# Optimization experiments

Measured on AMD Instinct MI355X. Metric: run time of the kernel, lower is better.

## Reference

```python
import jax, jax.numpy as jnp
import numpy as np

B, N, D, E = 4, 1024, 1024, 8
TOP_N = 2
THRESHOLD = 0.2
EPS = 1e-9
CAP_FACTOR = 2.0
MIN_EXPERT_CAPACITY = 4
H = int(D * 4 * 2 / 3)  # GEGLU hidden = 2730


def setup_inputs() -> dict:
    key = jax.random.key(0)
    ks = jax.random.split(key, 8)
    u = lambda k, shape, fan: jax.random.uniform(k, shape, jnp.float32, -1.0, 1.0) * (fan ** -0.5)
    return {
        "x": jax.random.normal(ks[0], (B, N, D), jnp.float32),
        "route_probs": jax.random.uniform(ks[1], (TOP_N, B, N), jnp.float32),
        "gate_w": u(ks[2], (D, E), D),
        "w1": u(ks[3], (E, D, 2 * H), 2 * H),
        "b1": u(ks[4], (E, 2 * H), 2 * H),
        "mult_bias": jnp.ones((E, H), jnp.float32),
        "w2": u(ks[5], (E, H, D), D),
        "b2": u(ks[6], (E, D), D),
    }


def reference(x, route_probs, gate_w, w1, b1, mult_bias, w2, b2):
    b, n, d = x.shape
    e = gate_w.shape[1]
    cap = max(min(n, int(n * CAP_FACTOR / e)), MIN_EXPERT_CAPACITY)  # 256

    # ---- top-n gating ----
    logits = jnp.einsum('bnd,de->bne', x, gate_w)
    raw_gates = jax.nn.softmax(logits, axis=-1)
    gate_vals, gate_idx = jax.lax.top_k(raw_gates, TOP_N)          # [b,n,k]
    gate_vals = jnp.moveaxis(gate_vals, -1, 0)                      # [k,b,n]
    gate_idx = jnp.moveaxis(gate_idx, -1, 0)                        # [k,b,n]
    one_hot_idx = jax.nn.one_hot(gate_idx, e, dtype=x.dtype)        # [k,b,n,e]

    denom = jnp.clip(gate_vals.sum(axis=0, keepdims=True), EPS)
    gate_vals = gate_vals / denom

    # route to expert k>0 with prob min(1, gate/threshold); expert 0 always routed
    should_route = route_probs < (gate_vals / THRESHOLD)
    should_route = should_route.at[0].set(True)
    mask = one_hot_idx * should_route[..., None].astype(x.dtype)    # [k,b,n,e]

    # exclusive cumsum over sequence dim -> position within each expert
    mask_cumsum = jnp.cumsum(mask, axis=2) - mask                   # [k,b,n,e]

    positions, masks = [], []
    prev_count = jnp.zeros((b, 1, e), x.dtype)
    for k in range(TOP_N):  # small fixed loop over top-n
        pos_e = (mask_cumsum[k] + prev_count) * mask[k]             # [b,n,e]
        mk = mask[k] * (pos_e < float(cap)).astype(x.dtype)
        prev_count = prev_count + mk.sum(axis=1, keepdims=True)
        positions.append(pos_e.sum(axis=-1))                        # [b,n]
        masks.append(mk)
    positions = jnp.stack(positions)                                # [k,b,n]
    mask = jnp.stack(masks)                                         # [k,b,n,e]

    mask_flat = mask.sum(axis=-1)                                   # [k,b,n] in {0,1}
    gates = gate_vals * mask_flat
    pos_one_hot = jax.nn.one_hot(positions.astype(jnp.int32), cap, dtype=x.dtype)  # [k,b,n,c]

    # combine tensor [b,n,e,c]; dispatch is its boolean support
    combine = jnp.einsum('kbn,kbne,kbnc->bnec', gates * mask_flat, one_hot_idx, pos_one_hot)
    dispatch = (combine > 0).astype(x.dtype)

    # ---- dispatch tokens to experts ----
    xe = jnp.einsum('bnd,bnec->ebcd', x, dispatch)                  # [e,b,c,d]

    # ---- per-expert GEGLU FFN (grouped GEMM) ----
    h = jnp.einsum('ebcd,edf->ebcf', xe, w1) + b1[:, None, None, :]
    val, gate = jnp.split(h, 2, axis=-1)
    act = jax.nn.gelu(gate, approximate=False) * val * mult_bias[:, None, None, :]
    out_e = jnp.einsum('ebch,ehd->ebcd', act, w2) + b2[:, None, None, :]

    # ---- combine ----
    out = jnp.einsum('ebcd,bnec->bnd', out_e, combine)
    return out


if __name__ == '__main__':
    inp = setup_inputs()
    o = reference(**inp)
    print(o.shape, o.dtype)
```

## Files before the change

### kernel.cpp

```cpp
#include <hip/hip_runtime.h>
#include <hip/hip_bf16.h>
#include <math.h>

#define B_ 4
#define N_ 1024
#define D_ 1024
#define E_ 8
#define H_ 2730
#define H2_ 5460
#define CAP_ 256
#define NTOK 4096
#define NSLOT 8192
#define NKT1 16
#define NKT2 43
#define NFG 22

typedef __attribute__((ext_vector_type(8))) short short8;
typedef __attribute__((ext_vector_type(4))) float f32x4;

__device__ __forceinline__ unsigned short f2bf(float f) {
    __hip_bfloat16 h = __float2bfloat16(f);
    return *reinterpret_cast<unsigned short*>(&h);
}
__device__ __forceinline__ float bf2f(unsigned short u) {
    unsigned x = ((unsigned)u) << 16;
    union { unsigned u; float f; } c; c.u = x; return c.f;
}

#define GLL16(g, l)                                                          \
    __builtin_amdgcn_global_load_lds(                                        \
        (const __attribute__((address_space(1))) void*)(g),                  \
        (__attribute__((address_space(3))) void*)(l), 16, 0, 0)

#define VMCNT4() asm volatile("s_waitcnt vmcnt(4)" ::: "memory")
#define VMCNT3() asm volatile("s_waitcnt vmcnt(3)" ::: "memory")
#define VMCNT0() asm volatile("s_waitcnt vmcnt(0)" ::: "memory")
#define SBAR()   __builtin_amdgcn_s_barrier()
#define SCHEDB() __builtin_amdgcn_sched_barrier(0)
#define MFMA16(a, b, c) __builtin_amdgcn_mfma_f32_16x16x32_bf16((a), (b), (c), 0, 0, 0)


__global__ __launch_bounds__(256) void k_cvt1(const float* __restrict__ w1,
                                              unsigned short* __restrict__ w1p) {
    const int fg = blockIdx.x;
    const int kt = blockIdx.y;
    const int e  = blockIdx.z;
    const float* w1e = w1 + (size_t)e * D_ * H2_;
    unsigned short* dst = w1p + (((size_t)((e * NFG + fg) * NKT1 + kt)) << 14);
#pragma unroll
    for (int i = 0; i < 8; ++i) {
        const int o = i * 256 + threadIdx.x;
        const int l = o & 63, n16 = (o >> 6) & 15, k32 = o >> 10;
        const int f = fg * 128 + ((n16 & 7) << 4) + (l & 15);
        const int k = kt * 64 + (k32 << 5) + ((l >> 4) << 3);
        ushort4 r0 = {0, 0, 0, 0}, r1 = {0, 0, 0, 0};
        if (f < H_) {
            const float* s = w1e + (size_t)k * H2_ + (n16 >= 8 ? H_ : 0) + f;
            r0.x = f2bf(s[0]);
            r0.y = f2bf(s[(size_t)H2_]);
            r0.z = f2bf(s[(size_t)2 * H2_]);
            r0.w = f2bf(s[(size_t)3 * H2_]);
            r1.x = f2bf(s[(size_t)4 * H2_]);
            r1.y = f2bf(s[(size_t)5 * H2_]);
            r1.z = f2bf(s[(size_t)6 * H2_]);
            r1.w = f2bf(s[(size_t)7 * H2_]);
        }
        *reinterpret_cast<ushort4*>(dst + (size_t)o * 8) = r0;
        *reinterpret_cast<ushort4*>(dst + (size_t)o * 8 + 4) = r1;
    }
}

__global__ __launch_bounds__(256) void k_cvt2(const float* __restrict__ w2,
                                              unsigned short* __restrict__ w2p) {
    const int kt = blockIdx.x;
    const int nt = blockIdx.y;
    const int e  = blockIdx.z;
    const float* w2e = w2 + (size_t)e * H_ * D_;
    unsigned short* dst = w2p + (((size_t)((e * 8 + nt) * NKT2 + kt)) << 13);
#pragma unroll
    for (int i = 0; i < 4; ++i) {
        const int o = i * 256 + threadIdx.x;
        const int l = o & 63, n16 = (o >> 6) & 7, k32 = o >> 9;
        const int d = nt * 128 + (n16 << 4) + (l & 15);
        const int f = kt * 64 + (k32 << 5) + ((l >> 4) << 3);
        const float* s = w2e + (size_t)f * D_ + d;
        ushort4 r0, r1;
        r0.x = (f + 0 < H_) ? f2bf(s[0]) : 0;
        r0.y = (f + 1 < H_) ? f2bf(s[(size_t)D_]) : 0;
        r0.z = (f + 2 < H_) ? f2bf(s[(size_t)2 * D_]) : 0;
        r0.w = (f + 3 < H_) ? f2bf(s[(size_t)3 * D_]) : 0;
        r1.x = (f + 4 < H_) ? f2bf(s[(size_t)4 * D_]) : 0;
        r1.y = (f + 5 < H_) ? f2bf(s[(size_t)5 * D_]) : 0;
        r1.z = (f + 6 < H_) ? f2bf(s[(size_t)6 * D_]) : 0;
        r1.w = (f + 7 < H_) ? f2bf(s[(size_t)7 * D_]) : 0;
        *reinterpret_cast<ushort4*>(dst + (size_t)o * 8) = r0;
        *reinterpret_cast<ushort4*>(dst + (size_t)o * 8 + 4) = r1;
    }
}

__global__ __launch_bounds__(256) void k_gate(const float* __restrict__ x,
                                              const float* __restrict__ route,
                                              const float* __restrict__ gw,
                                              int* __restrict__ tokE,
                                              float* __restrict__ tokG,
                                              int* __restrict__ tokR) {
    const int wave = threadIdx.x >> 6, lane = threadIdx.x & 63;
    const int t = blockIdx.x * 4 + wave;
    float acc[E_];
#pragma unroll
    for (int e = 0; e < E_; ++e) acc[e] = 0.f;
    const float* xr = x + (size_t)t * D_;
    for (int d = lane; d < D_; d += 64) {
        float xv = xr[d];
        const float* g = gw + d * E_;
#pragma unroll
        for (int e = 0; e < E_; ++e) acc[e] = fmaf(xv, g[e], acc[e]);
    }
#pragma unroll
    for (int e = 0; e < E_; ++e) {
#pragma unroll
        for (int off = 32; off; off >>= 1) acc[e] += __shfl_xor(acc[e], off);
    }
    if (lane == 0) {
        float m = acc[0];
#pragma unroll
        for (int e = 1; e < E_; ++e) m = fmaxf(m, acc[e]);
        float p[E_]; float s = 0.f;
#pragma unroll
        for (int e = 0; e < E_; ++e) { p[e] = expf(acc[e] - m); s += p[e]; }
        int i0 = 0; float v0 = p[0];
#pragma unroll
        for (int e = 1; e < E_; ++e) if (p[e] > v0) { v0 = p[e]; i0 = e; }
        int i1 = (i0 == 0) ? 1 : 0; float v1 = p[i1];
#pragma unroll
        for (int e = 0; e < E_; ++e) if (e != i0 && p[e] > v1) { v1 = p[e]; i1 = e; }
        float p0 = v0 / s, p1 = v1 / s;
        float denom = fmaxf(p0 + p1, 1e-9f);
        float g0 = p0 / denom, g1 = p1 / denom;
        int r1 = route[NTOK + t] < (g1 / 0.2f);
        tokE[t] = i0; tokE[NTOK + t] = i1;
        tokG[t] = g0; tokG[NTOK + t] = g1;
        tokR[t] = r1;
    }
}

__global__ __launch_bounds__(256) void k_pos(const int* __restrict__ tokE,
                                             const float* __restrict__ tokG,
                                             const int* __restrict__ tokR,
                                             int* __restrict__ sot,
                                             int* __restrict__ tos) {
    const int e = blockIdx.x & 7, b = blockIdx.x >> 3;
    const int t = threadIdx.x;
    __shared__ int sc[256];
    const int base_bt = b * N_ + t * 4;
    int m0[4], m1[4];
    int c0 = 0, c1 = 0;
#pragma unroll
    for (int i = 0; i < 4; ++i) {
        int bt = base_bt + i;
        m0[i] = (tokE[bt] == e) ? 1 : 0;
        m1[i] = ((tokE[NTOK + bt] == e) && tokR[bt]) ? 1 : 0;
        c0 += m0[i]; c1 += m1[i];
    }
    int packed = c0 | (c1 << 16);
    sc[t] = packed;
    __syncthreads();
    for (int off = 1; off < 256; off <<= 1) {
        int v = (t >= off) ? sc[t - off] : 0;
        __syncthreads();
        sc[t] += v;
        __syncthreads();
    }
    int incl = sc[t];
    int total = sc[255];
    int excl = incl - packed;
    int base0 = excl & 0xffff;
    int base1 = excl >> 16;
    int kept0 = min(total & 0xffff, CAP_);
#pragma unroll
    for (int i = 0; i < 4; ++i) {
        int bt = base_bt + i;
        if (m0[i]) {
            int pos = base0++;
            if (pos < CAP_ && tokG[bt] > 0.f) {
                int s = ((e * B_ + b) << 8) + pos;
                sot[bt] = s;
                tos[s] = bt;
            }
        }
        if (m1[i]) {
            int pos = (base1++) + kept0;
            if (pos < CAP_ && tokG[NTOK + bt] > 0.f) {
                int s = ((e * B_ + b) << 8) + pos;
                sot[NTOK + bt] = s;
                tos[s] = bt;
            }
        }
    }
}

__global__ __launch_bounds__(256) void k_disp(const float* __restrict__ x,
                                              const int* __restrict__ tos,
                                              unsigned short* __restrict__ xeP) {
    const int t = threadIdx.x;
    const int s = blockIdx.x * 2 + (t >> 7);
    const int q = t & 127;
    const int bt = tos[s];
    const int kt = q >> 3, k32 = (q >> 2) & 1, kq = q & 3;
    const int lane = (kq << 4) | (s & 15);
    const int m16 = (s >> 4) & 15;
    const int sgrp = s >> 8;
    unsigned short* dst = xeP + (((size_t)(sgrp * NKT1 + kt)) << 14) + (k32 << 13) + (m16 << 9) + lane * 8;
    ushort4 r0 = {0, 0, 0, 0}, r1 = {0, 0, 0, 0};
    if (bt >= 0) {
        const float4 v0 = *reinterpret_cast<const float4*>(x + ((size_t)bt << 10) + q * 8);
        const float4 v1 = *reinterpret_cast<const float4*>(x + ((size_t)bt << 10) + q * 8 + 4);
        r0.x = f2bf(v0.x); r0.y = f2bf(v0.y); r0.z = f2bf(v0.z); r0.w = f2bf(v0.w);
        r1.x = f2bf(v1.x); r1.y = f2bf(v1.y); r1.z = f2bf(v1.z); r1.w = f2bf(v1.w);
    }
    *reinterpret_cast<ushort4*>(dst) = r0;
    *reinterpret_cast<ushort4*>(dst + 4) = r1;
}

#define LDF(BUF, idx) (*reinterpret_cast<const short8*>(&BUF[(idx) * 512 + lane8]))

#define FFN1_MM03(AF0, AF1, AF2, AF3)                                         \
    do {                                                                      \
        acc[0][0]=MFMA16(AF0,bf0,acc[0][0]); acc[0][1]=MFMA16(AF0,bf1,acc[0][1]); \
        acc[0][2]=MFMA16(AF0,bf2,acc[0][2]); acc[0][3]=MFMA16(AF0,bf3,acc[0][3]); \
        acc[1][0]=MFMA16(AF1,bf0,acc[1][0]); acc[1][1]=MFMA16(AF1,bf1,acc[1][1]); \
        acc[1][2]=MFMA16(AF1,bf2,acc[1][2]); acc[1][3]=MFMA16(AF1,bf3,acc[1][3]); \
        acc[2][0]=MFMA16(AF2,bf0,acc[2][0]); acc[2][1]=MFMA16(AF2,bf1,acc[2][1]); \
        acc[2][2]=MFMA16(AF2,bf2,acc[2][2]); acc[2][3]=MFMA16(AF2,bf3,acc[2][3]); \
        acc[3][0]=MFMA16(AF3,bf0,acc[3][0]); acc[3][1]=MFMA16(AF3,bf1,acc[3][1]); \
        acc[3][2]=MFMA16(AF3,bf2,acc[3][2]); acc[3][3]=MFMA16(AF3,bf3,acc[3][3]); \
    } while (0)
#define FFN1_MM47(AF0, AF1, AF2, AF3)                                         \
    do {                                                                      \
        acc[4][0]=MFMA16(AF0,bf0,acc[4][0]); acc[4][1]=MFMA16(AF0,bf1,acc[4][1]); \
        acc[4][2]=MFMA16(AF0,bf2,acc[4][2]); acc[4][3]=MFMA16(AF0,bf3,acc[4][3]); \
        acc[5][0]=MFMA16(AF1,bf0,acc[5][0]); acc[5][1]=MFMA16(AF1,bf1,acc[5][1]); \
        acc[5][2]=MFMA16(AF1,bf2,acc[5][2]); acc[5][3]=MFMA16(AF1,bf3,acc[5][3]); \
        acc[6][0]=MFMA16(AF2,bf0,acc[6][0]); acc[6][1]=MFMA16(AF2,bf1,acc[6][1]); \
        acc[6][2]=MFMA16(AF2,bf2,acc[6][2]); acc[6][3]=MFMA16(AF2,bf3,acc[6][3]); \
        acc[7][0]=MFMA16(AF3,bf0,acc[7][0]); acc[7][1]=MFMA16(AF3,bf1,acc[7][1]); \
        acc[7][2]=MFMA16(AF3,bf2,acc[7][2]); acc[7][3]=MFMA16(AF3,bf3,acc[7][3]); \
    } while (0)

#define FFN1_KT(ARD, BRD, AWR, BWR, KTN, PF)                                  \
    do {                                                                      \
        const unsigned short* asn = abase + ((size_t)(KTN) << 14);            \
        const unsigned short* bsn = bbase + ((size_t)(KTN) << 14);            \
        short8 af0, af1, af2, af3, bf0, bf1, bf2, bf3;                        \
        SCHEDB(); VMCNT4(); SBAR(); SCHEDB();                                 \
        if (PF) {                                                             \
            GLL16(asn + woff + lane8, (char*)&AWR[woff]);                     \
            GLL16(asn + woff + 512 + lane8, (char*)&AWR[woff + 512]);         \
        }                                                                     \
        bf0 = LDF(BRD, bn0); bf1 = LDF(BRD, bn0 + 1);                         \
        bf2 = LDF(BRD, bn0 + 8); bf3 = LDF(BRD, bn0 + 9);                     \
        af0 = LDF(ARD, am0 + 0); af1 = LDF(ARD, am0 + 1);                     \
        af2 = LDF(ARD, am0 + 2); af3 = LDF(ARD, am0 + 3);                     \
        __builtin_amdgcn_s_setprio(1);                                        \
        FFN1_MM03(af0, af1, af2, af3);                                        \
        __builtin_amdgcn_s_setprio(0);                                        \
        if (PF) {                                                             \
            GLL16(bsn + woff + lane8, (char*)&BWR[woff]);                     \
            GLL16(bsn + woff + 512 + lane8, (char*)&BWR[woff + 512]);         \
        }                                                                     \
        af0 = LDF(ARD, am0 + 4); af1 = LDF(ARD, am0 + 5);                     \
        af2 = LDF(ARD, am0 + 6); af3 = LDF(ARD, am0 + 7);                     \
        __builtin_amdgcn_s_setprio(1);                                        \
        FFN1_MM47(af0, af1, af2, af3);                                        \
        __builtin_amdgcn_s_setprio(0);                                        \
        SCHEDB(); if (PF) { VMCNT4(); } else { VMCNT0(); } SBAR(); SCHEDB();  \
        if (PF) {                                                             \
            GLL16(asn + 8192 + woff + lane8, (char*)&AWR[8192 + woff]);       \
            GLL16(asn + 8192 + woff + 512 + lane8, (char*)&AWR[8192 + woff + 512]); \
        }                                                                     \
        bf0 = LDF(BRD, 16 + bn0); bf1 = LDF(BRD, 16 + bn0 + 1);               \
        bf2 = LDF(BRD, 16 + bn0 + 8); bf3 = LDF(BRD, 16 + bn0 + 9);           \
        af0 = LDF(ARD, 16 + am0 + 0); af1 = LDF(ARD, 16 + am0 + 1);           \
        af2 = LDF(ARD, 16 + am0 + 2); af3 = LDF(ARD, 16 + am0 + 3);           \
        __builtin_amdgcn_s_setprio(1);                                        \
        FFN1_MM03(af0, af1, af2, af3);                                        \
        __builtin_amdgcn_s_setprio(0);                                        \
        if (PF) {                                                             \
            GLL16(bsn + 8192 + woff + lane8, (char*)&BWR[8192 + woff]);       \
            GLL16(bsn + 8192 + woff + 512 + lane8, (char*)&BWR[8192 + woff + 512]); \
        }                                                                     \
        af0 = LDF(ARD, 16 + am0 + 4); af1 = LDF(ARD, 16 + am0 + 5);           \
        af2 = LDF(ARD, 16 + am0 + 6); af3 = LDF(ARD, 16 + am0 + 7);           \
        __builtin_amdgcn_s_setprio(1);                                        \
        FFN1_MM47(af0, af1, af2, af3);                                        \
        __builtin_amdgcn_s_setprio(0);                                        \
    } while (0)

__global__ __launch_bounds__(512) void k_ffn1(const unsigned short* __restrict__ xeP,
                                              const unsigned short* __restrict__ w1p,
                                              const float* __restrict__ b1,
                                              const float* __restrict__ mbias,
                                              unsigned short* __restrict__ actP) {
    const int wg = blockIdx.x;
    const int e = wg & 7;
    const int rem = wg >> 3;
    const int fg = rem >> 2;
    const int rt = rem & 3;
    const int sgrp = e * 4 + rt;

    __shared__ unsigned short Ab0[16384];
    __shared__ unsigned short Bb0[16384];
    __shared__ unsigned short Ab1[16384];
    __shared__ unsigned short Bb1[16384];

    const int tid = threadIdx.x, lane = tid & 63, w = tid >> 6;
    const int wm = w >> 2, wn = w & 3;
    const int lane8 = lane * 8;
    const int woff = w * 1024;
    const int am0 = wm * 8, bn0 = wn * 2;

    const unsigned short* abase = xeP + ((size_t)(sgrp * NKT1) << 14);
    const unsigned short* bbase = w1p + ((size_t)((e * NFG + fg) * NKT1) << 14);

    f32x4 acc[8][4];
#pragma unroll
    for (int i = 0; i < 8; ++i)
#pragma unroll
        for (int j = 0; j < 4; ++j) acc[i][j] = (f32x4)(0.f);

    GLL16(abase + woff + lane8, (char*)&Ab0[woff]);
    GLL16(abase + woff + 512 + lane8, (char*)&Ab0[woff + 512]);
    GLL16(bbase + woff + lane8, (char*)&Bb0[woff]);
    GLL16(bbase + woff + 512 + lane8, (char*)&Bb0[woff + 512]);
    GLL16(abase + 8192 + woff + lane8, (char*)&Ab0[8192 + woff]);
    GLL16(abase + 8192 + woff + 512 + lane8, (char*)&Ab0[8192 + woff + 512]);
    GLL16(bbase + 8192 + woff + lane8, (char*)&Bb0[8192 + woff]);
    GLL16(bbase + 8192 + woff + 512 + lane8, (char*)&Bb0[8192 + woff + 512]);

    for (int kt = 0; kt < NKT1; kt += 2) {
        FFN1_KT(Ab0, Bb0, Ab1, Bb1, kt + 1, 1);
        FFN1_KT(Ab1, Bb1, Ab0, Bb0, kt + 2, (kt + 2) < NKT1);
    }

    const float* b1e = b1 + (size_t)e * H2_;
    const float* mbe = mbias + (size_t)e * H_;
    const int colL = lane & 15, rq4 = (lane >> 4) * 4;
#pragma unroll
    for (int mi = 0; mi < 8; ++mi) {
        const int Rl = wm * 128 + mi * 16 + rq4;
#pragma unroll
        for (int vi = 0; vi < 2; ++vi) {
            const int f = fg * 128 + wn * 32 + vi * 16 + colL;
            if (f >= NKT2 * 64) continue;
            const bool real = f < H_;
            const float bv = real ? b1e[f] : 0.f;
            const float bg = real ? b1e[H_ + f] : 0.f;
            const float mv = real ? mbe[f] : 0.f;
            const int ktf = f >> 6, k32f = (f >> 5) & 1;
            const int lhi = ((f >> 3) & 3) << 4;
            const int bb = f & 7;
            const size_t cbase = ((size_t)(sgrp * NKT2 + ktf) << 14) + (k32f << 13);
#pragma unroll
            for (int j = 0; j < 4; ++j) {
                const int R = Rl + j;
                float a = 0.f;
                if (real) {
                    const float val = acc[mi][vi][j] + bv;
                    const float gt  = acc[mi][2 + vi][j] + bg;
                    a = 0.5f * gt * (1.f + erff(gt * 0.70710678118654752f)) * val * mv;
                }
                actP[cbase + ((R >> 4) << 9) + (size_t)((lhi | (R & 15)) * 8 + bb)] = f2bf(a);
            }
        }
    }
}

#define FFN2_MM03(AF0, AF1, AF2, AF3)                                         \
    do {                                                                      \
        acc[0][0]=MFMA16(AF0,bf0,acc[0][0]); acc[0][1]=MFMA16(AF0,bf1,acc[0][1]); \
        acc[1][0]=MFMA16(AF1,bf0,acc[1][0]); acc[1][1]=MFMA16(AF1,bf1,acc[1][1]); \
        acc[2][0]=MFMA16(AF2,bf0,acc[2][0]); acc[2][1]=MFMA16(AF2,bf1,acc[2][1]); \
        acc[3][0]=MFMA16(AF3,bf0,acc[3][0]); acc[3][1]=MFMA16(AF3,bf1,acc[3][1]); \
    } while (0)
#define FFN2_MM47(AF0, AF1, AF2, AF3)                                         \
    do {                                                                      \
        acc[4][0]=MFMA16(AF0,bf0,acc[4][0]); acc[4][1]=MFMA16(AF0,bf1,acc[4][1]); \
        acc[5][0]=MFMA16(AF1,bf0,acc[5][0]); acc[5][1]=MFMA16(AF1,bf1,acc[5][1]); \
        acc[6][0]=MFMA16(AF2,bf0,acc[6][0]); acc[6][1]=MFMA16(AF2,bf1,acc[6][1]); \
        acc[7][0]=MFMA16(AF3,bf0,acc[7][0]); acc[7][1]=MFMA16(AF3,bf1,acc[7][1]); \
    } while (0)

#define FFN2_KT(ARD, BRD, AWR, BWR, KTN, PF)                                  \
    do {                                                                      \
        const unsigned short* asn = abase + ((size_t)(KTN) << 14);            \
        const unsigned short* bsn = bbase + ((size_t)(KTN) << 13);            \
        short8 af0, af1, af2, af3, bf0, bf1;                                  \
        SCHEDB(); VMCNT3(); SBAR(); SCHEDB();                                 \
        if (PF) {                                                             \
            GLL16(asn + woff + lane8, (char*)&AWR[woff]);                     \
            GLL16(asn + woff + 512 + lane8, (char*)&AWR[woff + 512]);         \
        }                                                                     \
        bf0 = LDF(BRD, bn0); bf1 = LDF(BRD, bn0 + 1);                         \
        af0 = LDF(ARD, am0 + 0); af1 = LDF(ARD, am0 + 1);                     \
        af2 = LDF(ARD, am0 + 2); af3 = LDF(ARD, am0 + 3);                     \
        __builtin_amdgcn_s_setprio(1);                                        \
        FFN2_MM03(af0, af1, af2, af3);                                        \
        __builtin_amdgcn_s_setprio(0);                                        \
        if (PF) { GLL16(bsn + woffb + lane8, (char*)&BWR[woffb]); }           \
        af0 = LDF(ARD, am0 + 4); af1 = LDF(ARD, am0 + 5);                     \
        af2 = LDF(ARD, am0 + 6); af3 = LDF(ARD, am0 + 7);                     \
        __builtin_amdgcn_s_setprio(1);                                        \
        FFN2_MM47(af0, af1, af2, af3);                                        \
        __builtin_amdgcn_s_setprio(0);                                        \
        SCHEDB(); if (PF) { VMCNT3(); } else { VMCNT0(); } SBAR(); SCHEDB();  \
        if (PF) {                                                             \
            GLL16(asn + 8192 + woff + lane8, (char*)&AWR[8192 + woff]);       \
            GLL16(asn + 8192 + woff + 512 + lane8, (char*)&AWR[8192 + woff + 512]); \
        }                                                                     \
        bf0 = LDF(BRD, 8 + bn0); bf1 = LDF(BRD, 8 + bn0 + 1);                 \
        af0 = LDF(ARD, 16 + am0 + 0); af1 = LDF(ARD, 16 + am0 + 1);           \
        af2 = LDF(ARD, 16 + am0 + 2); af3 = LDF(ARD, 16 + am0 + 3);           \
        __builtin_amdgcn_s_setprio(1);                                        \
        FFN2_MM03(af0, af1, af2, af3);                                        \
        __builtin_amdgcn_s_setprio(0);                                        \
        if (PF) { GLL16(bsn + 4096 + woffb + lane8, (char*)&BWR[4096 + woffb]); } \
        af0 = LDF(ARD, 16 + am0 + 4); af1 = LDF(ARD, 16 + am0 + 5);           \
        af2 = LDF(ARD, 16 + am0 + 6); af3 = LDF(ARD, 16 + am0 + 7);           \
        __builtin_amdgcn_s_setprio(1);                                        \
        FFN2_MM47(af0, af1, af2, af3);                                        \
        __builtin_amdgcn_s_setprio(0);                                        \
    } while (0)

__global__ __launch_bounds__(512) void k_ffn2(const unsigned short* __restrict__ actP,
                                              const unsigned short* __restrict__ w2p,
                                              const float* __restrict__ b2,
                                              unsigned short* __restrict__ oute) {
    const int wg = blockIdx.x;
    const int e = wg & 7;
    const int rem = wg >> 3;
    const int nt = rem >> 2;
    const int mt = rem & 3;
    const int sgrp = e * 4 + mt;

    __shared__ unsigned short Ab0[16384];
    __shared__ unsigned short Bb0[8192];
    __shared__ unsigned short Ab1[16384];
    __shared__ unsigned short Bb1[8192];

    const int tid = threadIdx.x, lane = tid & 63, w = tid >> 6;
    const int wm = w >> 2, wn = w & 3;
    const int lane8 = lane * 8;
    const int woff = w * 1024;
    const int woffb = w * 512;
    const int am0 = wm * 8, bn0 = wn * 2;

    const unsigned short* abase = actP + ((size_t)(sgrp * NKT2) << 14);
    const unsigned short* bbase = w2p + ((size_t)((e * 8 + nt) * NKT2) << 13);

    f32x4 acc[8][2];
#pragma unroll
    for (int i = 0; i < 8; ++i)
#pragma unroll
        for (int j = 0; j < 2; ++j) acc[i][j] = (f32x4)(0.f);

    GLL16(abase + woff + lane8, (char*)&Ab0[woff]);
    GLL16(abase + woff + 512 + lane8, (char*)&Ab0[woff + 512]);
    GLL16(bbase + woffb + lane8, (char*)&Bb0[woffb]);
    GLL16(abase + 8192 + woff + lane8, (char*)&Ab0[8192 + woff]);
    GLL16(abase + 8192 + woff + 512 + lane8, (char*)&Ab0[8192 + woff + 512]);
    GLL16(bbase + 4096 + woffb + lane8, (char*)&Bb0[4096 + woffb]);

    for (int kt = 0; kt < NKT2 - 1; kt += 2) {
        FFN2_KT(Ab0, Bb0, Ab1, Bb1, kt + 1, 1);
        FFN2_KT(Ab1, Bb1, Ab0, Bb0, kt + 2, (kt + 2) < NKT2);
    }
    FFN2_KT(Ab0, Bb0, Ab1, Bb1, NKT2, 0);

    const float* b2e = b2 + (size_t)e * D_;
    const int colL = lane & 15, rq4 = (lane >> 4) * 4;
#pragma unroll
    for (int mi = 0; mi < 8; ++mi) {
#pragma unroll
        for (int vi = 0; vi < 2; ++vi) {
            const int d = nt * 128 + wn * 32 + vi * 16 + colL;
            const float bb2 = b2e[d];
#pragma unroll
            for (int j = 0; j < 4; ++j) {
                const int R = mt * 256 + wm * 128 + mi * 16 + rq4 + j;
                oute[((size_t)(e * 1024 + R) << 10) + d] = f2bf(acc[mi][vi][j] + bb2);
            }
        }
    }
}

__global__ __launch_bounds__(256) void k_comb(const unsigned short* __restrict__ oute,
                                              const int* __restrict__ sot,
                                              const float* __restrict__ tokG,
                                              float* __restrict__ out) {
    const int bt = blockIdx.x;
    const int t = threadIdx.x;
    const int s0 = sot[bt], s1 = sot[NTOK + bt];
    const float g0 = tokG[bt], g1 = tokG[NTOK + bt];
    float r0 = 0.f, r1 = 0.f, r2 = 0.f, r3 = 0.f;
    if (s0 >= 0) {
        const ushort4 v = *reinterpret_cast<const ushort4*>(oute + ((size_t)s0 << 10) + t * 4);
        r0 += g0 * bf2f(v.x); r1 += g0 * bf2f(v.y); r2 += g0 * bf2f(v.z); r3 += g0 * bf2f(v.w);
    }
    if (s1 >= 0) {
        const ushort4 v = *reinterpret_cast<const ushort4*>(oute + ((size_t)s1 << 10) + t * 4);
        r0 += g1 * bf2f(v.x); r1 += g1 * bf2f(v.y); r2 += g1 * bf2f(v.z); r3 += g1 * bf2f(v.w);
    }
    float4 o; o.x = r0; o.y = r1; o.z = r2; o.w = r3;
    *reinterpret_cast<float4*>(out + ((size_t)bt << 10) + t * 4) = o;
}

extern "C" void kernel_launch(void* const* d_in, const int* in_sizes, int n_in,
                              void* d_out, int out_size, void* d_ws, size_t ws_size,
                              hipStream_t stream) {
    const float* x     = (const float*)d_in[0];
    const float* route = (const float*)d_in[1];
    const float* gw    = (const float*)d_in[2];
    const float* w1    = (const float*)d_in[3];
    const float* b1    = (const float*)d_in[4];
    const float* mb    = (const float*)d_in[5];
    const float* w2    = (const float*)d_in[6];
    const float* b2    = (const float*)d_in[7];
    float* out = (float*)d_out;

    char* ws = (char*)d_ws;
    int*   tokE = (int*)(ws + 0);
    float* tokG = (float*)(ws + 32768);
    int*   tokR = (int*)(ws + 65536);
    int*   sot  = (int*)(ws + 81920);
    int*   tos  = (int*)(ws + 114688);
    unsigned short* xeP  = (unsigned short*)(ws + 147456);
    unsigned short* actP = (unsigned short*)(ws + 16924672);
    unsigned short* w1p  = (unsigned short*)(ws + 62013440);
    unsigned short* w2p  = (unsigned short*)(ws + 62013440);
    unsigned short* oute = (unsigned short*)(ws + 107102208);

    hipMemsetAsync(sot, 0xFF, 65536, stream);

    k_cvt1<<<dim3(NFG, NKT1, 8), 256, 0, stream>>>(w1, w1p);
    k_gate<<<NTOK / 4, 256, 0, stream>>>(x, route, gw, tokE, tokG, tokR);
    k_pos<<<E_ * B_, 256, 0, stream>>>(tokE, tokG, tokR, sot, tos);
    k_disp<<<NSLOT / 2, 256, 0, stream>>>(x, tos, xeP);
    k_ffn1<<<704, 512, 0, stream>>>(xeP, w1p, b1, mb, actP);
    k_cvt2<<<dim3(NKT2, 8, 8), 256, 0, stream>>>(w2, w2p);
    k_ffn2<<<256, 512, 0, stream>>>(actP, w2p, b2, oute);
    k_comb<<<NTOK, 256, 0, stream>>>(oute, sot, tokG, out);
}
```

Measured before the change: 325.6 us.

## Restructure FFN GEMM k-loops with explicit barrier/lgkmcnt staging of LDS reads

Reorders both grouped-GEMM main loops so LDS fragment reads are issued before the global-to-LDS prefetches, then an explicit barrier plus lgkmcnt(0) wait precedes each MFMA cluster, in a ping-pong style schedule. The vmcnt wait and barrier move from the start of each tile to its end, with a prologue wait added. In FFN2 the two half-clusters are merged into one 16-MFMA block that loads all eight A fragments at once. This aims to overlap memory and compute across the 8 waves more predictably, at the cost of extra barriers and more live registers.

```diff
diff --git a/kernel.cpp b/kernel.cpp
--- a/kernel.cpp
+++ b/kernel.cpp
@@ -35,6 +35,7 @@
 #define VMCNT4() asm volatile("s_waitcnt vmcnt(4)" ::: "memory")
 #define VMCNT3() asm volatile("s_waitcnt vmcnt(3)" ::: "memory")
 #define VMCNT0() asm volatile("s_waitcnt vmcnt(0)" ::: "memory")
+#define LGKM0()  asm volatile("s_waitcnt lgkmcnt(0)" ::: "memory")
 #define SBAR()   __builtin_amdgcn_s_barrier()
 #define SCHEDB() __builtin_amdgcn_sched_barrier(0)
 #define MFMA16(a, b, c) __builtin_amdgcn_mfma_f32_16x16x32_bf16((a), (b), (c), 0, 0, 0)
@@ -247,53 +248,63 @@
         acc[7][2]=MFMA16(AF3,bf2,acc[7][2]); acc[7][3]=MFMA16(AF3,bf3,acc[7][3]); \
     } while (0)
 
-#define FFN1_KT(ARD, BRD, AWR, BWR, KTN, PF)                                  \
+#define FFN1_TILE(ARD, BRD, AWR, BWR, KTN, PF)                                \
     do {                                                                      \
         const unsigned short* asn = abase + ((size_t)(KTN) << 14);            \
         const unsigned short* bsn = bbase + ((size_t)(KTN) << 14);            \
         short8 af0, af1, af2, af3, bf0, bf1, bf2, bf3;                        \
-        SCHEDB(); VMCNT4(); SBAR(); SCHEDB();                                 \
+                                                          \
+        bf0 = LDF(BRD, bn0); bf1 = LDF(BRD, bn0 + 1);                         \
+        bf2 = LDF(BRD, bn0 + 8); bf3 = LDF(BRD, bn0 + 9);                     \
+        af0 = LDF(ARD, am0 + 0); af1 = LDF(ARD, am0 + 1);                     \
+        af2 = LDF(ARD, am0 + 2); af3 = LDF(ARD, am0 + 3);                     \
         if (PF) {                                                             \
             GLL16(asn + woff + lane8, (char*)&AWR[woff]);                     \
             GLL16(asn + woff + 512 + lane8, (char*)&AWR[woff + 512]);         \
         }                                                                     \
-        bf0 = LDF(BRD, bn0); bf1 = LDF(BRD, bn0 + 1);                         \
-        bf2 = LDF(BRD, bn0 + 8); bf3 = LDF(BRD, bn0 + 9);                     \
-        af0 = LDF(ARD, am0 + 0); af1 = LDF(ARD, am0 + 1);                     \
-        af2 = LDF(ARD, am0 + 2); af3 = LDF(ARD, am0 + 3);                     \
+        SBAR(); LGKM0(); SCHEDB();                                            \
         __builtin_amdgcn_s_setprio(1);                                        \
         FFN1_MM03(af0, af1, af2, af3);                                        \
         __builtin_amdgcn_s_setprio(0);                                        \
+        SBAR();                                                               \
+                                                          \
+        af0 = LDF(ARD, am0 + 4); af1 = LDF(ARD, am0 + 5);                     \
+        af2 = LDF(ARD, am0 + 6); af3 = LDF(ARD, am0 + 7);                     \
         if (PF) {                                                             \
             GLL16(bsn + woff + lane8, (char*)&BWR[woff]);                     \
             GLL16(bsn + woff + 512 + lane8, (char*)&BWR[woff + 512]);         \
         }                                                                     \
-        af0 = LDF(ARD, am0 + 4); af1 = LDF(ARD, am0 + 5);                     \
-        af2 = LDF(ARD, am0 + 6); af3 = LDF(ARD, am0 + 7);                     \
+        SBAR(); LGKM0(); SCHEDB();                                            \
         __builtin_amdgcn_s_setprio(1);                                        \
         FFN1_MM47(af0, af1, af2, af3);                                        \
         __builtin_amdgcn_s_setprio(0);                                        \
         SCHEDB(); if (PF) { VMCNT4(); } else { VMCNT0(); } SBAR(); SCHEDB();  \
+                                                          \
+        bf0 = LDF(BRD, 16 + bn0); bf1 = LDF(BRD, 16 + bn0 + 1);               \
+        bf2 = LDF(BRD, 16 + bn0 + 8); bf3 = LDF(BRD, 16 + bn0 + 9);           \
+        af0 = LDF(ARD, 16 + am0 + 0); af1 = LDF(ARD, 16 + am0 + 1);           \
+        af2 = LDF(ARD, 16 + am0 + 2); af3 = LDF(ARD, 16 + am0 + 3);           \
         if (PF) {                                                             \
             GLL16(asn + 8192 + woff + lane8, (char*)&AWR[8192 + woff]);       \
             GLL16(asn + 8192 + woff + 512 + lane8, (char*)&AWR[8192 + woff + 512]); \
         }                                                                     \
-        bf0 = LDF(BRD, 16 + bn0); bf1 = LDF(BRD, 16 + bn0 + 1);               \
-        bf2 = LDF(BRD, 16 + bn0 + 8); bf3 = LDF(BRD, 16 + bn0 + 9);           \
-        af0 = LDF(ARD, 16 + am0 + 0); af1 = LDF(ARD, 16 + am0 + 1);           \
-        af2 = LDF(ARD, 16 + am0 + 2); af3 = LDF(ARD, 16 + am0 + 3);           \
+        SBAR(); LGKM0(); SCHEDB();                                            \
         __builtin_amdgcn_s_setprio(1);                                        \
         FFN1_MM03(af0, af1, af2, af3);                                        \
         __builtin_amdgcn_s_setprio(0);                                        \
+        SBAR();                                                               \
+                                                          \
+        af0 = LDF(ARD, 16 + am0 + 4); af1 = LDF(ARD, 16 + am0 + 5);           \
+        af2 = LDF(ARD, 16 + am0 + 6); af3 = LDF(ARD, 16 + am0 + 7);           \
         if (PF) {                                                             \
             GLL16(bsn + 8192 + woff + lane8, (char*)&BWR[8192 + woff]);       \
             GLL16(bsn + 8192 + woff + 512 + lane8, (char*)&BWR[8192 + woff + 512]); \
         }                                                                     \
-        af0 = LDF(ARD, 16 + am0 + 4); af1 = LDF(ARD, 16 + am0 + 5);           \
-        af2 = LDF(ARD, 16 + am0 + 6); af3 = LDF(ARD, 16 + am0 + 7);           \
+        SBAR(); LGKM0(); SCHEDB();                                            \
         __builtin_amdgcn_s_setprio(1);                                        \
         FFN1_MM47(af0, af1, af2, af3);                                        \
         __builtin_amdgcn_s_setprio(0);                                        \
+        SCHEDB(); if (PF) { VMCNT4(); } else { VMCNT0(); } SBAR(); SCHEDB();  \
     } while (0)
 
 __global__ __launch_bounds__(512) void k_ffn1(const unsigned short* __restrict__ xeP,
@@ -336,10 +347,11 @@
     GLL16(abase + 8192 + woff + 512 + lane8, (char*)&Ab0[8192 + woff + 512]);
     GLL16(bbase + 8192 + woff + lane8, (char*)&Bb0[8192 + woff]);
     GLL16(bbase + 8192 + woff + 512 + lane8, (char*)&Bb0[8192 + woff + 512]);
+    SCHEDB(); VMCNT4(); SBAR(); SCHEDB();
 
     for (int kt = 0; kt < NKT1; kt += 2) {
-        FFN1_KT(Ab0, Bb0, Ab1, Bb1, kt + 1, 1);
-        FFN1_KT(Ab1, Bb1, Ab0, Bb0, kt + 2, (kt + 2) < NKT1);
+        FFN1_TILE(Ab0, Bb0, Ab1, Bb1, kt + 1, 1);
+        FFN1_TILE(Ab1, Bb1, Ab0, Bb0, kt + 2, (kt + 2) < NKT1);
     }
 
     const float* b1e = b1 + (size_t)e * H2_;
@@ -375,60 +387,55 @@
     }
 }
 
-#define FFN2_MM03(AF0, AF1, AF2, AF3)                                         \
+#define FFN2_MM(AF0, AF1, AF2, AF3, AF4, AF5, AF6, AF7)                       \
     do {                                                                      \
         acc[0][0]=MFMA16(AF0,bf0,acc[0][0]); acc[0][1]=MFMA16(AF0,bf1,acc[0][1]); \
         acc[1][0]=MFMA16(AF1,bf0,acc[1][0]); acc[1][1]=MFMA16(AF1,bf1,acc[1][1]); \
         acc[2][0]=MFMA16(AF2,bf0,acc[2][0]); acc[2][1]=MFMA16(AF2,bf1,acc[2][1]); \
         acc[3][0]=MFMA16(AF3,bf0,acc[3][0]); acc[3][1]=MFMA16(AF3,bf1,acc[3][1]); \
+        acc[4][0]=MFMA16(AF4,bf0,acc[4][0]); acc[4][1]=MFMA16(AF4,bf1,acc[4][1]); \
+        acc[5][0]=MFMA16(AF5,bf0,acc[5][0]); acc[5][1]=MFMA16(AF5,bf1,acc[5][1]); \
+        acc[6][0]=MFMA16(AF6,bf0,acc[6][0]); acc[6][1]=MFMA16(AF6,bf1,acc[6][1]); \
+        acc[7][0]=MFMA16(AF7,bf0,acc[7][0]); acc[7][1]=MFMA16(AF7,bf1,acc[7][1]); \
     } while (0)
-#define FFN2_MM47(AF0, AF1, AF2, AF3)                                         \
-    do {                                                                      \
-        acc[4][0]=MFMA16(AF0,bf0,acc[4][0]); acc[4][1]=MFMA16(AF0,bf1,acc[4][1]); \
-        acc[5][0]=MFMA16(AF1,bf0,acc[5][0]); acc[5][1]=MFMA16(AF1,bf1,acc[5][1]); \
-        acc[6][0]=MFMA16(AF2,bf0,acc[6][0]); acc[6][1]=MFMA16(AF2,bf1,acc[6][1]); \
-        acc[7][0]=MFMA16(AF3,bf0,acc[7][0]); acc[7][1]=MFMA16(AF3,bf1,acc[7][1]); \
-    } while (0)
-
-#define FFN2_KT(ARD, BRD, AWR, BWR, KTN, PF)                                  \
+
+#define FFN2_TILE(ARD, BRD, AWR, BWR, KTN, PF)                                \
     do {                                                                      \
         const unsigned short* asn = abase + ((size_t)(KTN) << 14);            \
         const unsigned short* bsn = bbase + ((size_t)(KTN) << 13);            \
-        short8 af0, af1, af2, af3, bf0, bf1;                                  \
-        SCHEDB(); VMCNT3(); SBAR(); SCHEDB();                                 \
+        short8 af0, af1, af2, af3, af4, af5, af6, af7, bf0, bf1;              \
+                                                         \
+        bf0 = LDF(BRD, bn0); bf1 = LDF(BRD, bn0 + 1);                         \
+        af0 = LDF(ARD, am0 + 0); af1 = LDF(ARD, am0 + 1);                     \
+        af2 = LDF(ARD, am0 + 2); af3 = LDF(ARD, am0 + 3);                     \
+        af4 = LDF(ARD, am0 + 4); af5 = LDF(ARD, am0 + 5);                     \
+        af6 = LDF(ARD, am0 + 6); af7 = LDF(ARD, am0 + 7);                     \
         if (PF) {                                                             \
             GLL16(asn + woff + lane8, (char*)&AWR[woff]);                     \
             GLL16(asn + woff + 512 + lane8, (char*)&AWR[woff + 512]);         \
+            GLL16(bsn + woffb + lane8, (char*)&BWR[woffb]);                   \
         }                                                                     \
-        bf0 = LDF(BRD, bn0); bf1 = LDF(BRD, bn0 + 1);                         \
-        af0 = LDF(ARD, am0 + 0); af1 = LDF(ARD, am0 + 1);                     \
-        af2 = LDF(ARD, am0 + 2); af3 = LDF(ARD, am0 + 3);                     \
+        SBAR(); LGKM0(); SCHEDB();                                            \
         __builtin_amdgcn_s_setprio(1);                                        \
-        FFN2_MM03(af0, af1, af2, af3);                                        \
-        __builtin_amdgcn_s_setprio(0);                                        \
-        if (PF) { GLL16(bsn + woffb + lane8, (char*)&BWR[woffb]); }           \
-        af0 = LDF(ARD, am0 + 4); af1 = LDF(ARD, am0 + 5);                     \
-        af2 = LDF(ARD, am0 + 6); af3 = LDF(ARD, am0 + 7);                     \
-        __builtin_amdgcn_s_setprio(1);                                        \
-        FFN2_MM47(af0, af1, af2, af3);                                        \
+        FFN2_MM(af0, af1, af2, af3, af4, af5, af6, af7);                      \
         __builtin_amdgcn_s_setprio(0);                                        \
         SCHEDB(); if (PF) { VMCNT3(); } else { VMCNT0(); } SBAR(); SCHEDB();  \
+                                                         \
+        bf0 = LDF(BRD, 8 + bn0); bf1 = LDF(BRD, 8 + bn0 + 1);                 \
+        af0 = LDF(ARD, 16 + am0 + 0); af1 = LDF(ARD, 16 + am0 + 1);           \
+        af2 = LDF(ARD, 16 + am0 + 2); af3 = LDF(ARD, 16 + am0 + 3);           \
+        af4 = LDF(ARD, 16 + am0 + 4); af5 = LDF(ARD, 16 + am0 + 5);           \
+        af6 = LDF(ARD, 16 + am0 + 6); af7 = LDF(ARD, 16 + am0 + 7);           \
         if (PF) {                                                             \
             GLL16(asn + 8192 + woff + lane8, (char*)&AWR[8192 + woff]);       \
             GLL16(asn + 8192 + woff + 512 + lane8, (char*)&AWR[8192 + woff + 512]); \
+            GLL16(bsn + 4096 + woffb + lane8, (char*)&BWR[4096 + woffb]);     \
         }                                                                     \
-        bf0 = LDF(BRD, 8 + bn0); bf1 = LDF(BRD, 8 + bn0 + 1);                 \
-        af0 = LDF(ARD, 16 + am0 + 0); af1 = LDF(ARD, 16 + am0 + 1);           \
-        af2 = LDF(ARD, 16 + am0 + 2); af3 = LDF(ARD, 16 + am0 + 3);           \
+        SBAR(); LGKM0(); SCHEDB();                                            \
         __builtin_amdgcn_s_setprio(1);                                        \
-        FFN2_MM03(af0, af1, af2, af3);                                        \
+        FFN2_MM(af0, af1, af2, af3, af4, af5, af6, af7);                      \
         __builtin_amdgcn_s_setprio(0);                                        \
-        if (PF) { GLL16(bsn + 4096 + woffb + lane8, (char*)&BWR[4096 + woffb]); } \
-        af0 = LDF(ARD, 16 + am0 + 4); af1 = LDF(ARD, 16 + am0 + 5);           \
-        af2 = LDF(ARD, 16 + am0 + 6); af3 = LDF(ARD, 16 + am0 + 7);           \
-        __builtin_amdgcn_s_setprio(1);                                        \
-        FFN2_MM47(af0, af1, af2, af3);                                        \
-        __builtin_amdgcn_s_setprio(0);                                        \
+        SCHEDB(); if (PF) { VMCNT3(); } else { VMCNT0(); } SBAR(); SCHEDB();  \
     } while (0)
 
 __global__ __launch_bounds__(512) void k_ffn2(const unsigned short* __restrict__ actP,
@@ -469,12 +476,13 @@
     GLL16(abase + 8192 + woff + lane8, (char*)&Ab0[8192 + woff]);
     GLL16(abase + 8192 + woff + 512 + lane8, (char*)&Ab0[8192 + woff + 512]);
     GLL16(bbase + 4096 + woffb + lane8, (char*)&Bb0[4096 + woffb]);
+    SCHEDB(); VMCNT3(); SBAR(); SCHEDB();
 
     for (int kt = 0; kt < NKT2 - 1; kt += 2) {
-        FFN2_KT(Ab0, Bb0, Ab1, Bb1, kt + 1, 1);
-        FFN2_KT(Ab1, Bb1, Ab0, Bb0, kt + 2, (kt + 2) < NKT2);
-    }
-    FFN2_KT(Ab0, Bb0, Ab1, Bb1, NKT2, 0);
+        FFN2_TILE(Ab0, Bb0, Ab1, Bb1, kt + 1, 1);
+        FFN2_TILE(Ab1, Bb1, Ab0, Bb0, kt + 2, (kt + 2) < NKT2);
+    }
+    FFN2_TILE(Ab0, Bb0, Ab1, Bb1, NKT2, 0);
 
     const float* b2e = b2 + (size_t)e * D_;
     const int colL = lane & 15, rq4 = (lane >> 4) * 4;
```

Result: slower. 339.8 us (+4.4%).
